# Kernel tuning notes

Hardware: AMD Instinct MI355X
Metric: run time of the kernel (lower is better)

## Reference

```python
import jax, jax.numpy as jnp
import numpy as np

SKS = 3  # small kernel size
PAD = (SKS - 1) // 2
GROUPS = 8


def setup_inputs() -> dict:
    key = jax.random.key(0)
    k1, k2 = jax.random.split(key)
    B, C, H, W = 8, 64, 128, 128
    x = jax.random.normal(k1, (B, C, H, W), dtype=jnp.float32)
    # dynamic per-pixel aggregation weights, shared across Cg within each group
    w = jax.random.normal(k2, (B, GROUPS, 1, SKS * SKS, H, W), dtype=jnp.float32)
    return {"x": x, "w": w}


def reference(x, w):
    # Faithful to: patches = unfold(x, k=3, pad=1).view(B, g, Cg, 9, H, W); (patches * w).sum(3)
    # Implemented as a fused shift-multiply-accumulate over the 9 fixed taps,
    B, C, H, W = x.shape
    g = w.shape[1]
    Cg = C // g
    xp = jnp.pad(x, ((0, 0), (0, 0), (PAD, PAD), (PAD, PAD)))
    xp = xp.reshape(B, g, Cg, H + 2 * PAD, W + 2 * PAD)
    out = jnp.zeros((B, g, Cg, H, W), dtype=x.dtype)
    for k in range(SKS * SKS):  # fixed 9 taps, unrolled at trace time
        ki, kj = divmod(k, SKS)  # unfold orders kernel positions row-major
        out = out + xp[:, :, :, ki:ki + H, kj:kj + W] * w[:, :, :, k]
    return out.reshape(B, C, H, W)
```

## Files before the change

kernel.cpp:

```cpp
#include <hip/hip_runtime.h>
#include <hip/hip_bf16.h>

#define BATCH 8
#define CHN   64
#define GRP   8
#define CG    8
#define HH    128
#define WW    128
#define HW    (HH * WW)

__global__ __launch_bounds__(256, 3) void ska_small_kernel(
    const float* __restrict__ x,
    const float* __restrict__ wgt,
    float* __restrict__ out)
{
    int tid = blockIdx.x * blockDim.x + threadIdx.x;
    int q  = tid & 31;
    int w0 = q * 4;
    int h2 = (tid >> 5) & 63;
    int g  = (tid >> 11) & 7;
    int b  = tid >> 14;

    const int h0 = h2 * 2;
    const int h1 = h0 + 1;

    const float* wbase = wgt + ((size_t)(b * GRP + g) * 9) * HW + (size_t)h0 * WW + w0;
    float4 wk0[9], wk1[9];
#pragma unroll
    for (int k = 0; k < 9; ++k) {
        wk0[k] = *(const float4*)(wbase + (size_t)k * HW);
        wk1[k] = *(const float4*)(wbase + (size_t)k * HW + WW);
    }

    const float m_top = (h0 > 0)      ? 1.0f : 0.0f;
    const float m_bot = (h1 < HH - 1) ? 1.0f : 0.0f;
#pragma unroll
    for (int j = 0; j < 3; ++j) {
        wk0[j].x     *= m_top; wk0[j].y     *= m_top; wk0[j].z     *= m_top; wk0[j].w     *= m_top;
        wk1[6 + j].x *= m_bot; wk1[6 + j].y *= m_bot; wk1[6 + j].z *= m_bot; wk1[6 + j].w *= m_bot;
    }

    const float mL = (q > 0)  ? 1.0f : 0.0f;
    const float mR = (q < 31) ? 1.0f : 0.0f;

    const int hm = (h0 > 0)      ? h0 - 1 : h0;
    const int hp = (h1 < HH - 1) ? h1 + 1 : h1;

    const float* xbase = x   + (size_t)(b * CHN + g * CG) * HW + w0;
    float*       obase = out + (size_t)(b * CHN + g * CG) * HW + (size_t)h0 * WW + w0;

#pragma unroll
    for (int cg = 0; cg < CG; ++cg) {
        const float* xc = xbase + (size_t)cg * HW;
        float4 rm = *(const float4*)(xc + (size_t)hm * WW);
        float4 r0 = *(const float4*)(xc + (size_t)h0 * WW);
        float4 r1 = *(const float4*)(xc + (size_t)h1 * WW);
        float4 rp = *(const float4*)(xc + (size_t)hp * WW);

        float win[4][6];
        win[0][1] = rm.x; win[0][2] = rm.y; win[0][3] = rm.z; win[0][4] = rm.w;
        win[1][1] = r0.x; win[1][2] = r0.y; win[1][3] = r0.z; win[1][4] = r0.w;
        win[2][1] = r1.x; win[2][2] = r1.y; win[2][3] = r1.z; win[2][4] = r1.w;
        win[3][1] = rp.x; win[3][2] = rp.y; win[3][3] = rp.z; win[3][4] = rp.w;
        win[0][0] = __shfl_up(rm.w, 1) * mL;
        win[1][0] = __shfl_up(r0.w, 1) * mL;
        win[2][0] = __shfl_up(r1.w, 1) * mL;
        win[3][0] = __shfl_up(rp.w, 1) * mL;
        win[0][5] = __shfl_down(rm.x, 1) * mR;
        win[1][5] = __shfl_down(r0.x, 1) * mR;
        win[2][5] = __shfl_down(r1.x, 1) * mR;
        win[3][5] = __shfl_down(rp.x, 1) * mR;

        float4 acc0 = make_float4(0.f, 0.f, 0.f, 0.f);
        float4 acc1 = make_float4(0.f, 0.f, 0.f, 0.f);
#pragma unroll
        for (int ki = 0; ki < 3; ++ki) {
#pragma unroll
            for (int kj = 0; kj < 3; ++kj) {
                const float4 wv0 = wk0[ki * 3 + kj];
                const float4 wv1 = wk1[ki * 3 + kj];
                acc0.x = fmaf(win[ki    ][0 + kj], wv0.x, acc0.x);
                acc0.y = fmaf(win[ki    ][1 + kj], wv0.y, acc0.y);
                acc0.z = fmaf(win[ki    ][2 + kj], wv0.z, acc0.z);
                acc0.w = fmaf(win[ki    ][3 + kj], wv0.w, acc0.w);
                acc1.x = fmaf(win[ki + 1][0 + kj], wv1.x, acc1.x);
                acc1.y = fmaf(win[ki + 1][1 + kj], wv1.y, acc1.y);
                acc1.z = fmaf(win[ki + 1][2 + kj], wv1.z, acc1.z);
                acc1.w = fmaf(win[ki + 1][3 + kj], wv1.w, acc1.w);
            }
        }

        *(float4*)(obase + (size_t)cg * HW)      = acc0;
        *(float4*)(obase + (size_t)cg * HW + WW) = acc1;
    }
}

extern "C" void kernel_launch(void* const* d_in, const int* in_sizes, int n_in,
                              void* d_out, int out_size, void* d_ws, size_t ws_size,
                              hipStream_t stream) {
    const float* x = (const float*)d_in[0];
    const float* w = (const float*)d_in[1];
    float* out = (float*)d_out;

    const int total = BATCH * GRP * (HH / 2) * (WW / 4);
    const int block = 256;
    const int grid = total / block;
    ska_small_kernel<<<grid, block, 0, stream>>>(x, w, out);
}
```

Measured before the change: 104.9 us.

## Parallelize channels across warps and share weights via LDS

Measured after the change: 105.5 us. No clear change (+0.6%).

```diff
diff --git a/kernel.cpp b/kernel.cpp
--- a/kernel.cpp
+++ b/kernel.cpp
@@ -1,5 +1,4 @@
 #include <hip/hip_runtime.h>
-#include <hip/hip_bf16.h>
 
 #define BATCH 8
 #define CHN   64
@@ -9,90 +8,87 @@
 #define WW    128
 #define HW    (HH * WW)
 
-__global__ __launch_bounds__(256, 3) void ska_small_kernel(
+__global__ __launch_bounds__(256, 6) void ska_small_kernel(
     const float* __restrict__ x,
     const float* __restrict__ wgt,
     float* __restrict__ out)
 {
-    int tid = blockIdx.x * blockDim.x + threadIdx.x;
-    int q  = tid & 31;
-    int w0 = q * 4;
-    int h2 = (tid >> 5) & 63;
-    int g  = (tid >> 11) & 7;
-    int b  = tid >> 14;
+    __shared__ __align__(16) float lds_w[9][2][WW];
 
+    const int bid = blockIdx.x;
+    const int h2 = bid & 63;
+    const int g  = (bid >> 6) & 7;
+    const int b  = bid >> 9;
     const int h0 = h2 * 2;
     const int h1 = h0 + 1;
 
-    const float* wbase = wgt + ((size_t)(b * GRP + g) * 9) * HW + (size_t)h0 * WW + w0;
-    float4 wk0[9], wk1[9];
+    const int t  = threadIdx.x;
+    const int q  = t & 31;
+    const int cg = t >> 5;
+    const int w0 = q * 4;
+
+    const int hm = (h0 > 0)      ? h0 - 1 : h0;
+    const int hp = (h1 < HH - 1) ? h1 + 1 : h1;
+
+    const float* xc = x + (size_t)(b * CHN + g * CG + cg) * HW + w0;
+    const float4 rm = *(const float4*)(xc + (size_t)hm * WW);
+    const float4 r0 = *(const float4*)(xc + (size_t)h0 * WW);
+    const float4 r1 = *(const float4*)(xc + (size_t)h1 * WW);
+    const float4 rp = *(const float4*)(xc + (size_t)hp * WW);
+
+    {
+        const float* wsrc = wgt + ((size_t)(b * GRP + g) * 9) * HW + (size_t)h0 * WW;
+        const int  r    = t >> 7;
+        const bool ktop = (h0 == 0)      && (r == 0);
+        const bool kbot = (h1 == HH - 1) && (r == 1);
 #pragma unroll
-    for (int k = 0; k < 9; ++k) {
-        wk0[k] = *(const float4*)(wbase + (size_t)k * HW);
-        wk1[k] = *(const float4*)(wbase + (size_t)k * HW + WW);
+        for (int k = 0; k < 9; ++k) {
+            float v = wsrc[(size_t)k * HW + t];
+            if ((ktop && k < 3) || (kbot && k >= 6)) v = 0.f;
+            ((float*)lds_w)[k * 256 + t] = v;
+        }
     }
-
-    const float m_top = (h0 > 0)      ? 1.0f : 0.0f;
-    const float m_bot = (h1 < HH - 1) ? 1.0f : 0.0f;
-#pragma unroll
-    for (int j = 0; j < 3; ++j) {
-        wk0[j].x     *= m_top; wk0[j].y     *= m_top; wk0[j].z     *= m_top; wk0[j].w     *= m_top;
-        wk1[6 + j].x *= m_bot; wk1[6 + j].y *= m_bot; wk1[6 + j].z *= m_bot; wk1[6 + j].w *= m_bot;
-    }
+    __syncthreads();
 
     const float mL = (q > 0)  ? 1.0f : 0.0f;
     const float mR = (q < 31) ? 1.0f : 0.0f;
 
-    const int hm = (h0 > 0)      ? h0 - 1 : h0;
-    const int hp = (h1 < HH - 1) ? h1 + 1 : h1;
+    float win[4][6];
+    win[0][1] = rm.x; win[0][2] = rm.y; win[0][3] = rm.z; win[0][4] = rm.w;
+    win[1][1] = r0.x; win[1][2] = r0.y; win[1][3] = r0.z; win[1][4] = r0.w;
+    win[2][1] = r1.x; win[2][2] = r1.y; win[2][3] = r1.z; win[2][4] = r1.w;
+    win[3][1] = rp.x; win[3][2] = rp.y; win[3][3] = rp.z; win[3][4] = rp.w;
+    win[0][0] = __shfl_up(rm.w, 1) * mL;
+    win[1][0] = __shfl_up(r0.w, 1) * mL;
+    win[2][0] = __shfl_up(r1.w, 1) * mL;
+    win[3][0] = __shfl_up(rp.w, 1) * mL;
+    win[0][5] = __shfl_down(rm.x, 1) * mR;
+    win[1][5] = __shfl_down(r0.x, 1) * mR;
+    win[2][5] = __shfl_down(r1.x, 1) * mR;
+    win[3][5] = __shfl_down(rp.x, 1) * mR;
 
-    const float* xbase = x   + (size_t)(b * CHN + g * CG) * HW + w0;
-    float*       obase = out + (size_t)(b * CHN + g * CG) * HW + (size_t)h0 * WW + w0;
+    float4 acc0 = make_float4(0.f, 0.f, 0.f, 0.f);
+    float4 acc1 = make_float4(0.f, 0.f, 0.f, 0.f);
+#pragma unroll
+    for (int ki = 0; ki < 3; ++ki) {
+#pragma unroll
+        for (int kj = 0; kj < 3; ++kj) {
+            const float4 wv0 = *(const float4*)&lds_w[ki * 3 + kj][0][w0];
+            const float4 wv1 = *(const float4*)&lds_w[ki * 3 + kj][1][w0];
+            acc0.x = fmaf(win[ki    ][0 + kj], wv0.x, acc0.x);
+            acc0.y = fmaf(win[ki    ][1 + kj], wv0.y, acc0.y);
+            acc0.z = fmaf(win[ki    ][2 + kj], wv0.z, acc0.z);
+            acc0.w = fmaf(win[ki    ][3 + kj], wv0.w, acc0.w);
+            acc1.x = fmaf(win[ki + 1][0 + kj], wv1.x, acc1.x);
+            acc1.y = fmaf(win[ki + 1][1 + kj], wv1.y, acc1.y);
+            acc1.z = fmaf(win[ki + 1][2 + kj], wv1.z, acc1.z);
+            acc1.w = fmaf(win[ki + 1][3 + kj], wv1.w, acc1.w);
+        }
+    }
 
-#pragma unroll
-    for (int cg = 0; cg < CG; ++cg) {
-        const float* xc = xbase + (size_t)cg * HW;
-        float4 rm = *(const float4*)(xc + (size_t)hm * WW);
-        float4 r0 = *(const float4*)(xc + (size_t)h0 * WW);
-        float4 r1 = *(const float4*)(xc + (size_t)h1 * WW);
-        float4 rp = *(const float4*)(xc + (size_t)hp * WW);
-
-        float win[4][6];
-        win[0][1] = rm.x; win[0][2] = rm.y; win[0][3] = rm.z; win[0][4] = rm.w;
-        win[1][1] = r0.x; win[1][2] = r0.y; win[1][3] = r0.z; win[1][4] = r0.w;
-        win[2][1] = r1.x; win[2][2] = r1.y; win[2][3] = r1.z; win[2][4] = r1.w;
-        win[3][1] = rp.x; win[3][2] = rp.y; win[3][3] = rp.z; win[3][4] = rp.w;
-        win[0][0] = __shfl_up(rm.w, 1) * mL;
-        win[1][0] = __shfl_up(r0.w, 1) * mL;
-        win[2][0] = __shfl_up(r1.w, 1) * mL;
-        win[3][0] = __shfl_up(rp.w, 1) * mL;
-        win[0][5] = __shfl_down(rm.x, 1) * mR;
-        win[1][5] = __shfl_down(r0.x, 1) * mR;
-        win[2][5] = __shfl_down(r1.x, 1) * mR;
-        win[3][5] = __shfl_down(rp.x, 1) * mR;
-
-        float4 acc0 = make_float4(0.f, 0.f, 0.f, 0.f);
-        float4 acc1 = make_float4(0.f, 0.f, 0.f, 0.f);
-#pragma unroll
-        for (int ki = 0; ki < 3; ++ki) {
-#pragma unroll
-            for (int kj = 0; kj < 3; ++kj) {
-                const float4 wv0 = wk0[ki * 3 + kj];
-                const float4 wv1 = wk1[ki * 3 + kj];
-                acc0.x = fmaf(win[ki    ][0 + kj], wv0.x, acc0.x);
-                acc0.y = fmaf(win[ki    ][1 + kj], wv0.y, acc0.y);
-                acc0.z = fmaf(win[ki    ][2 + kj], wv0.z, acc0.z);
-                acc0.w = fmaf(win[ki    ][3 + kj], wv0.w, acc0.w);
-                acc1.x = fmaf(win[ki + 1][0 + kj], wv1.x, acc1.x);
-                acc1.y = fmaf(win[ki + 1][1 + kj], wv1.y, acc1.y);
-                acc1.z = fmaf(win[ki + 1][2 + kj], wv1.z, acc1.z);
-                acc1.w = fmaf(win[ki + 1][3 + kj], wv1.w, acc1.w);
-            }
-        }
-
-        *(float4*)(obase + (size_t)cg * HW)      = acc0;
-        *(float4*)(obase + (size_t)cg * HW + WW) = acc1;
-    }
+    float* oc = out + (size_t)(b * CHN + g * CG + cg) * HW + (size_t)h0 * WW + w0;
+    *(float4*)(oc)      = acc0;
+    *(float4*)(oc + WW) = acc1;
 }
 
 extern "C" void kernel_launch(void* const* d_in, const int* in_sizes, int n_in,
@@ -102,8 +98,6 @@
     const float* w = (const float*)d_in[1];
     float* out = (float*)d_out;
 
-    const int total = BATCH * GRP * (HH / 2) * (WW / 4);
-    const int block = 256;
-    const int grid = total / block;
-    ska_small_kernel<<<grid, block, 0, stream>>>(x, w, out);
+    const int grid = BATCH * GRP * (HH / 2);
+    ska_small_kernel<<<grid, 256, 0, stream>>>(x, w, out);
 }
```
